# Optimization experiments

Hardware: AMD Instinct MI355X
Metric: run time of the kernel (lower is better)

## Reference

```python
import jax, jax.numpy as jnp
import numpy as np

N_NODES = 50000
N_EDGES = 150000
EMB = 64
IN_DIM = 32
LN_EPS = 1e-5


def setup_inputs() -> dict:
    key = jax.random.key(0)
    k1, k2, k3, k4 = jax.random.split(key, 4)
    h = jax.random.normal(k1, (N_NODES, EMB), dtype=jnp.float32)
    edge_attr = jax.random.normal(k2, (N_EDGES, IN_DIM), dtype=jnp.float32)
    edge_index = jax.random.randint(k3, (2, N_EDGES), 0, N_NODES, dtype=jnp.int64)
    # xavier_uniform for [EMB*EMB, IN_DIM] weight
    limit = float(np.sqrt(6.0 / (EMB * EMB + IN_DIM)))
    W = jax.random.uniform(k4, (EMB * EMB, IN_DIM), dtype=jnp.float32,
                           minval=-limit, maxval=limit)
    b = jnp.zeros((EMB * EMB,), dtype=jnp.float32)
    gamma = jnp.ones((EMB,), dtype=jnp.float32)
    beta = jnp.zeros((EMB,), dtype=jnp.float32)
    return {"h": h, "edge_attr": edge_attr, "W": W, "b": b,
            "gamma": gamma, "beta": beta, "edge_index": edge_index}


def reference(h, edge_attr, W, b, gamma, beta, edge_index):
    M = edge_attr.shape[0]
    E = h.shape[1]
    # per-edge transform matrix from edge features: [M, E, E]
    m = (edge_attr @ W.T + b).reshape(M, E, E)
    # gather target-node features and apply per-edge matvec: [M, E]
    h_j = h[edge_index[1]]
    msg = jnp.einsum('mef,mf->me', m, h_j)
    # scatter-add messages to source nodes
    aggr = jax.ops.segment_sum(msg, edge_index[0], num_segments=h.shape[0])
    # residual + LayerNorm
    x = h + aggr
    mu = jnp.mean(x, axis=-1, keepdims=True)
    var = jnp.mean(jnp.square(x - mu), axis=-1, keepdims=True)
    y = (x - mu) * jax.lax.rsqrt(var + LN_EPS)
    return y * gamma + beta
```

## Files before the change

kernel.cpp:

```cpp
#include <hip/hip_runtime.h>
#include <math.h>

#define N_NODES 50000
#define N_EDGES 150000
#define LN_EPS 1e-5f

#define BM 128
#define WM 64

typedef _Float16 f16x8 __attribute__((ext_vector_type(8)));
typedef float    f32x4 __attribute__((ext_vector_type(4)));

__global__ void prep_kernel(const float* __restrict__ W, const float* __restrict__ b,
                            _Float16* __restrict__ WtF) {
    int tid = blockIdx.x * 256 + threadIdx.x;
    if (tid >= 66 * 4 * 64 * 8) return;
    int i  = tid & 7;
    int l  = (tid >> 3) & 63;
    int nb = (tid >> 9) & 3;
    int c  = tid >> 11;
    int k  = ((l >> 4) << 3) + i;
    int e  = nb * 16 + (l & 15);
    float v;
    if (c < 64) v = W[(e * 64 + c) * 32 + k];
    else        v = b[e * 64 + (c - 64) * 32 + k];
    WtF[tid] = (_Float16)v;
}

__global__ void init_kernel(const float* __restrict__ h, float* __restrict__ out) {
    int tid = blockIdx.x * 256 + threadIdx.x;
    ((float4*)out)[tid] = ((const float4*)h)[tid];
}

__launch_bounds__(128, 2)
__global__ void edge_kernel(const float* __restrict__ ea,
                            const float* __restrict__ h,
                            const int*   __restrict__ ei,
                            const f16x8* __restrict__ WtF,
                            float* __restrict__ out)
{
    __shared__ float s_hj[BM][68];
    __shared__ int   s_src[BM];

    const int t = threadIdx.x;
    const int m_base = blockIdx.x * BM;

    {
        int gm = m_base + t;
        if (gm < N_EDGES) {
            s_src[t] = ei[gm];
            const float4* hr = (const float4*)&h[(size_t)ei[N_EDGES + gm] * 64];
            #pragma unroll
            for (int j = 0; j < 16; ++j)
                *(float4*)&s_hj[t][j * 4] = hr[j];
        } else {
            s_src[t] = -1;
            float4 z = make_float4(0.f, 0.f, 0.f, 0.f);
            #pragma unroll
            for (int j = 0; j < 16; ++j)
                *(float4*)&s_hj[t][j * 4] = z;
        }
    }

    const int lane = t & 63;
    const int w    = t >> 6;
    const int r16  = lane & 15;
    const int g    = lane >> 4;
    const int k0   = g * 8;
    const int row0 = w * WM;

    float eareg[4][8];
    #pragma unroll
    for (int a = 0; a < 4; ++a) {
        int gm = m_base + row0 + a * 16 + r16;
        if (gm < N_EDGES) {
            float4 v0 = *(const float4*)&ea[(size_t)gm * 32 + k0];
            float4 v1 = *(const float4*)&ea[(size_t)gm * 32 + k0 + 4];
            eareg[a][0] = v0.x; eareg[a][1] = v0.y; eareg[a][2] = v0.z; eareg[a][3] = v0.w;
            eareg[a][4] = v1.x; eareg[a][5] = v1.y; eareg[a][6] = v1.z; eareg[a][7] = v1.w;
        } else {
            #pragma unroll
            for (int i = 0; i < 8; ++i) eareg[a][i] = 0.f;
        }
    }

    f32x4 acc[4][4];
    #pragma unroll
    for (int a = 0; a < 4; ++a)
        #pragma unroll
        for (int nb = 0; nb < 4; ++nb)
            acc[a][nb] = (f32x4){0.f, 0.f, 0.f, 0.f};

    __syncthreads();

    f16x8 bcur[4], bnxt[4];
    float hc[4], hn[4];
    #pragma unroll
    for (int nb = 0; nb < 4; ++nb) bcur[nb] = WtF[nb * 64 + lane];
    #pragma unroll
    for (int a = 0; a < 4; ++a) hc[a] = s_hj[row0 + a * 16 + r16][0];

    for (int c2 = 0; c2 < 32; ++c2) {
        const int c = 2 * c2;
        #pragma unroll
        for (int nb = 0; nb < 4; ++nb) bnxt[nb] = WtF[((c + 1) * 4 + nb) * 64 + lane];
        #pragma unroll
        for (int a = 0; a < 4; ++a) hn[a] = s_hj[row0 + a * 16 + r16][c + 1];
        #pragma unroll
        for (int a = 0; a < 4; ++a) {
            f16x8 va;
            #pragma unroll
            for (int i = 0; i < 4; ++i) {
                auto p = __builtin_amdgcn_cvt_pkrtz(eareg[a][2 * i]     * hc[a],
                                                    eareg[a][2 * i + 1] * hc[a]);
                va[2 * i]     = (_Float16)p[0];
                va[2 * i + 1] = (_Float16)p[1];
            }
            #pragma unroll
            for (int nb = 0; nb < 4; ++nb)
                acc[a][nb] = __builtin_amdgcn_mfma_f32_16x16x32_f16(va, bcur[nb], acc[a][nb], 0, 0, 0);
        }
        #pragma unroll
        for (int nb = 0; nb < 4; ++nb) bcur[nb] = WtF[((c + 2) * 4 + nb) * 64 + lane];
        {
            const int cn = (c + 2 < 64) ? (c + 2) : 0;
            #pragma unroll
            for (int a = 0; a < 4; ++a) hc[a] = s_hj[row0 + a * 16 + r16][cn];
        }
        #pragma unroll
        for (int a = 0; a < 4; ++a) {
            f16x8 va;
            #pragma unroll
            for (int i = 0; i < 4; ++i) {
                auto p = __builtin_amdgcn_cvt_pkrtz(eareg[a][2 * i]     * hn[a],
                                                    eareg[a][2 * i + 1] * hn[a]);
                va[2 * i]     = (_Float16)p[0];
                va[2 * i + 1] = (_Float16)p[1];
            }
            #pragma unroll
            for (int nb = 0; nb < 4; ++nb)
                acc[a][nb] = __builtin_amdgcn_mfma_f32_16x16x32_f16(va, bnxt[nb], acc[a][nb], 0, 0, 0);
        }
    }

    #pragma unroll
    for (int nb = 0; nb < 4; ++nb) bnxt[nb] = WtF[(65 * 4 + nb) * 64 + lane];
    #pragma unroll
    for (int a = 0; a < 4; ++a) {
        f16x8 va;
        #pragma unroll
        for (int i = 0; i < 8; ++i) va[i] = (_Float16)s_hj[row0 + a * 16 + r16][k0 + i];
        #pragma unroll
        for (int nb = 0; nb < 4; ++nb)
            acc[a][nb] = __builtin_amdgcn_mfma_f32_16x16x32_f16(va, bcur[nb], acc[a][nb], 0, 0, 0);
    }
    #pragma unroll
    for (int a = 0; a < 4; ++a) {
        f16x8 va;
        #pragma unroll
        for (int i = 0; i < 8; ++i) va[i] = (_Float16)s_hj[row0 + a * 16 + r16][32 + k0 + i];
        #pragma unroll
        for (int nb = 0; nb < 4; ++nb)
            acc[a][nb] = __builtin_amdgcn_mfma_f32_16x16x32_f16(va, bnxt[nb], acc[a][nb], 0, 0, 0);
    }

    #pragma unroll
    for (int a = 0; a < 4; ++a) {
        #pragma unroll
        for (int r = 0; r < 4; ++r) {
            int srcn = s_src[row0 + a * 16 + g * 4 + r];
            if (srcn >= 0) {
                #pragma unroll
                for (int nb = 0; nb < 4; ++nb)
                    atomicAdd(&out[(size_t)srcn * 64 + nb * 16 + r16], acc[a][nb][r]);
            }
        }
    }
}

__global__ void ln_kernel(const float* __restrict__ gamma, const float* __restrict__ beta,
                          float* __restrict__ out) {
    int row = blockIdx.x * 4 + (threadIdx.x >> 6);
    int lane = threadIdx.x & 63;
    if (row >= N_NODES) return;
    float x = out[row * 64 + lane];
    float s = x;
    #pragma unroll
    for (int o = 32; o; o >>= 1) s += __shfl_xor(s, o);
    float mu = s * (1.0f / 64.0f);
    float d = x - mu;
    float v = d * d;
    #pragma unroll
    for (int o = 32; o; o >>= 1) v += __shfl_xor(v, o);
    float var = v * (1.0f / 64.0f);
    float r = rsqrtf(var + LN_EPS);
    out[row * 64 + lane] = d * r * gamma[lane] + beta[lane];
}

extern "C" void kernel_launch(void* const* d_in, const int* in_sizes, int n_in,
                              void* d_out, int out_size, void* d_ws, size_t ws_size,
                              hipStream_t stream) {
    const float* h     = (const float*)d_in[0];
    const float* ea    = (const float*)d_in[1];
    const float* W     = (const float*)d_in[2];
    const float* b     = (const float*)d_in[3];
    const float* gamma = (const float*)d_in[4];
    const float* beta  = (const float*)d_in[5];
    const int*   ei    = (const int*)d_in[6];
    float* out = (float*)d_out;

    _Float16* WtF = (_Float16*)d_ws;

    prep_kernel<<<528, 256, 0, stream>>>(W, b, WtF);
    init_kernel<<<(N_NODES * 64 / 4 + 255) / 256, 256, 0, stream>>>(h, out);
    edge_kernel<<<(N_EDGES + BM - 1) / BM, 128, 0, stream>>>(ea, h, ei, (const f16x8*)WtF, out);
    ln_kernel<<<(N_NODES + 3) / 4, 256, 0, stream>>>(gamma, beta, out);
}
```

Measured before the change: 171.4 us.

## Split edge tile across four waves and triple-buffer weight fragment loads

The edge kernel now runs 256 threads per 128-edge block, so each wave covers 32 rows instead of 64. This halves the per-thread accumulator and edge-feature register footprint, and launch bounds are raised to allow four blocks per CU. Weight fragments are now prefetched three steps ahead instead of two, which gives more latency hiding per MFMA. The prep kernel is also vectorized to write 8-half vectors per thread. The tradeoff is that each weight fragment is now loaded by twice as many waves, doubling L2/L1 traffic for the shared B operand.

Measured after the change: 165.7 us. 3.3% less time.

```diff
diff --git a/kernel.cpp b/kernel.cpp
--- a/kernel.cpp
+++ b/kernel.cpp
@@ -6,25 +6,28 @@
 #define LN_EPS 1e-5f
 
 #define BM 128
-#define WM 64
+#define WM 32
 
 typedef _Float16 f16x8 __attribute__((ext_vector_type(8)));
 typedef float    f32x4 __attribute__((ext_vector_type(4)));
 
 __global__ void prep_kernel(const float* __restrict__ W, const float* __restrict__ b,
-                            _Float16* __restrict__ WtF) {
+                            f16x8* __restrict__ WtF) {
     int tid = blockIdx.x * 256 + threadIdx.x;
-    if (tid >= 66 * 4 * 64 * 8) return;
-    int i  = tid & 7;
-    int l  = (tid >> 3) & 63;
-    int nb = (tid >> 9) & 3;
-    int c  = tid >> 11;
-    int k  = ((l >> 4) << 3) + i;
+    if (tid >= 66 * 4 * 64) return;
+    int l  = tid & 63;
+    int nb = (tid >> 6) & 3;
+    int c  = tid >> 8;
+    int k0 = (l >> 4) << 3;
     int e  = nb * 16 + (l & 15);
-    float v;
-    if (c < 64) v = W[(e * 64 + c) * 32 + k];
-    else        v = b[e * 64 + (c - 64) * 32 + k];
-    WtF[tid] = (_Float16)v;
+    const float* src = (c < 64) ? &W[(e * 64 + c) * 32 + k0]
+                                : &b[e * 64 + (c - 64) * 32 + k0];
+    float4 v0 = *(const float4*)src;
+    float4 v1 = *(const float4*)(src + 4);
+    f16x8 o;
+    o[0] = (_Float16)v0.x; o[1] = (_Float16)v0.y; o[2] = (_Float16)v0.z; o[3] = (_Float16)v0.w;
+    o[4] = (_Float16)v1.x; o[5] = (_Float16)v1.y; o[6] = (_Float16)v1.z; o[7] = (_Float16)v1.w;
+    WtF[tid] = o;
 }
 
 __global__ void init_kernel(const float* __restrict__ h, float* __restrict__ out) {
@@ -32,7 +35,7 @@
     ((float4*)out)[tid] = ((const float4*)h)[tid];
 }
 
-__launch_bounds__(128, 2)
+__launch_bounds__(256, 4)
 __global__ void edge_kernel(const float* __restrict__ ea,
                             const float* __restrict__ h,
                             const int*   __restrict__ ei,
@@ -46,19 +49,21 @@
     const int m_base = blockIdx.x * BM;
 
     {
-        int gm = m_base + t;
+        int row  = t >> 1;
+        int half = t & 1;
+        int gm   = m_base + row;
         if (gm < N_EDGES) {
-            s_src[t] = ei[gm];
-            const float4* hr = (const float4*)&h[(size_t)ei[N_EDGES + gm] * 64];
-            #pragma unroll
-            for (int j = 0; j < 16; ++j)
-                *(float4*)&s_hj[t][j * 4] = hr[j];
+            if (half == 0) s_src[row] = ei[gm];
+            const float4* hr = (const float4*)&h[(size_t)ei[N_EDGES + gm] * 64 + half * 32];
+            #pragma unroll
+            for (int j = 0; j < 8; ++j)
+                *(float4*)&s_hj[row][half * 32 + j * 4] = hr[j];
         } else {
-            s_src[t] = -1;
+            if (half == 0) s_src[row] = -1;
             float4 z = make_float4(0.f, 0.f, 0.f, 0.f);
             #pragma unroll
-            for (int j = 0; j < 16; ++j)
-                *(float4*)&s_hj[t][j * 4] = z;
+            for (int j = 0; j < 8; ++j)
+                *(float4*)&s_hj[row][half * 32 + j * 4] = z;
         }
     }
 
@@ -68,10 +73,12 @@
     const int g    = lane >> 4;
     const int k0   = g * 8;
     const int row0 = w * WM;
-
-    float eareg[4][8];
-    #pragma unroll
-    for (int a = 0; a < 4; ++a) {
+    const int rA   = row0 + r16;
+    const int rB   = row0 + 16 + r16;
+
+    float eareg[2][8];
+    #pragma unroll
+    for (int a = 0; a < 2; ++a) {
         int gm = m_base + row0 + a * 16 + r16;
         if (gm < N_EDGES) {
             float4 v0 = *(const float4*)&ea[(size_t)gm * 32 + k0];
@@ -84,88 +91,110 @@
         }
     }
 
-    f32x4 acc[4][4];
-    #pragma unroll
-    for (int a = 0; a < 4; ++a)
+    f32x4 acc[2][4];
+    #pragma unroll
+    for (int a = 0; a < 2; ++a)
         #pragma unroll
         for (int nb = 0; nb < 4; ++nb)
             acc[a][nb] = (f32x4){0.f, 0.f, 0.f, 0.f};
 
     __syncthreads();
 
-    f16x8 bcur[4], bnxt[4];
-    float hc[4], hn[4];
-    #pragma unroll
-    for (int nb = 0; nb < 4; ++nb) bcur[nb] = WtF[nb * 64 + lane];
-    #pragma unroll
-    for (int a = 0; a < 4; ++a) hc[a] = s_hj[row0 + a * 16 + r16][0];
-
-    for (int c2 = 0; c2 < 32; ++c2) {
-        const int c = 2 * c2;
-        #pragma unroll
-        for (int nb = 0; nb < 4; ++nb) bnxt[nb] = WtF[((c + 1) * 4 + nb) * 64 + lane];
-        #pragma unroll
-        for (int a = 0; a < 4; ++a) hn[a] = s_hj[row0 + a * 16 + r16][c + 1];
-        #pragma unroll
-        for (int a = 0; a < 4; ++a) {
+    f16x8 b0[4], b1[4], b2[4];
+    #pragma unroll
+    for (int nb = 0; nb < 4; ++nb) b0[nb] = WtF[(0 * 4 + nb) * 64 + lane];
+    #pragma unroll
+    for (int nb = 0; nb < 4; ++nb) b1[nb] = WtF[(1 * 4 + nb) * 64 + lane];
+    #pragma unroll
+    for (int nb = 0; nb < 4; ++nb) b2[nb] = WtF[(2 * 4 + nb) * 64 + lane];
+
+    float hc0 = s_hj[rA][0];
+    float hc1 = s_hj[rB][0];
+
+    auto step = [&](int c, f16x8* bb, bool loadnext) {
+        float hn0 = 0.f, hn1 = 0.f;
+        if (loadnext) { hn0 = s_hj[rA][c + 1]; hn1 = s_hj[rB][c + 1]; }
+        {
             f16x8 va;
             #pragma unroll
             for (int i = 0; i < 4; ++i) {
-                auto p = __builtin_amdgcn_cvt_pkrtz(eareg[a][2 * i]     * hc[a],
-                                                    eareg[a][2 * i + 1] * hc[a]);
-                va[2 * i]     = (_Float16)p[0];
-                va[2 * i + 1] = (_Float16)p[1];
+                auto p = __builtin_amdgcn_cvt_pkrtz(eareg[0][2 * i]     * hc0,
+                                                    eareg[0][2 * i + 1] * hc0);
+                va[2 * i] = (_Float16)p[0]; va[2 * i + 1] = (_Float16)p[1];
             }
             #pragma unroll
             for (int nb = 0; nb < 4; ++nb)
-                acc[a][nb] = __builtin_amdgcn_mfma_f32_16x16x32_f16(va, bcur[nb], acc[a][nb], 0, 0, 0);
-        }
-        #pragma unroll
-        for (int nb = 0; nb < 4; ++nb) bcur[nb] = WtF[((c + 2) * 4 + nb) * 64 + lane];
+                acc[0][nb] = __builtin_amdgcn_mfma_f32_16x16x32_f16(va, bb[nb], acc[0][nb], 0, 0, 0);
+        }
         {
-            const int cn = (c + 2 < 64) ? (c + 2) : 0;
-            #pragma unroll
-            for (int a = 0; a < 4; ++a) hc[a] = s_hj[row0 + a * 16 + r16][cn];
-        }
-        #pragma unroll
-        for (int a = 0; a < 4; ++a) {
             f16x8 va;
             #pragma unroll
             for (int i = 0; i < 4; ++i) {
-                auto p = __builtin_amdgcn_cvt_pkrtz(eareg[a][2 * i]     * hn[a],
-                                                    eareg[a][2 * i + 1] * hn[a]);
-                va[2 * i]     = (_Float16)p[0];
-                va[2 * i + 1] = (_Float16)p[1];
+                auto p = __builtin_amdgcn_cvt_pkrtz(eareg[1][2 * i]     * hc1,
+                                                    eareg[1][2 * i + 1] * hc1);
+                va[2 * i] = (_Float16)p[0]; va[2 * i + 1] = (_Float16)p[1];
             }
             #pragma unroll
             for (int nb = 0; nb < 4; ++nb)
-                acc[a][nb] = __builtin_amdgcn_mfma_f32_16x16x32_f16(va, bnxt[nb], acc[a][nb], 0, 0, 0);
-        }
-    }
-
-    #pragma unroll
-    for (int nb = 0; nb < 4; ++nb) bnxt[nb] = WtF[(65 * 4 + nb) * 64 + lane];
-    #pragma unroll
-    for (int a = 0; a < 4; ++a) {
+                acc[1][nb] = __builtin_amdgcn_mfma_f32_16x16x32_f16(va, bb[nb], acc[1][nb], 0, 0, 0);
+        }
+        hc0 = hn0; hc1 = hn1;
+    };
+
+    for (int c = 0; c < 63; c += 3) {
+        step(c, b0, true);
+        #pragma unroll
+        for (int nb = 0; nb < 4; ++nb) b0[nb] = WtF[((c + 3) * 4 + nb) * 64 + lane];
+        step(c + 1, b1, true);
+        #pragma unroll
+        for (int nb = 0; nb < 4; ++nb) b1[nb] = WtF[((c + 4) * 4 + nb) * 64 + lane];
+        step(c + 2, b2, true);
+        #pragma unroll
+        for (int nb = 0; nb < 4; ++nb) b2[nb] = WtF[((c + 5) * 4 + nb) * 64 + lane];
+    }
+    step(63, b0, false);
+
+    {
         f16x8 va;
         #pragma unroll
-        for (int i = 0; i < 8; ++i) va[i] = (_Float16)s_hj[row0 + a * 16 + r16][k0 + i];
-        #pragma unroll
-        for (int nb = 0; nb < 4; ++nb)
-            acc[a][nb] = __builtin_amdgcn_mfma_f32_16x16x32_f16(va, bcur[nb], acc[a][nb], 0, 0, 0);
-    }
-    #pragma unroll
-    for (int a = 0; a < 4; ++a) {
+        for (int i = 0; i < 4; ++i) {
+            auto p = __builtin_amdgcn_cvt_pkrtz(s_hj[rA][k0 + 2 * i], s_hj[rA][k0 + 2 * i + 1]);
+            va[2 * i] = (_Float16)p[0]; va[2 * i + 1] = (_Float16)p[1];
+        }
+        #pragma unroll
+        for (int nb = 0; nb < 4; ++nb)
+            acc[0][nb] = __builtin_amdgcn_mfma_f32_16x16x32_f16(va, b1[nb], acc[0][nb], 0, 0, 0);
+        #pragma unroll
+        for (int i = 0; i < 4; ++i) {
+            auto p = __builtin_amdgcn_cvt_pkrtz(s_hj[rB][k0 + 2 * i], s_hj[rB][k0 + 2 * i + 1]);
+            va[2 * i] = (_Float16)p[0]; va[2 * i + 1] = (_Float16)p[1];
+        }
+        #pragma unroll
+        for (int nb = 0; nb < 4; ++nb)
+            acc[1][nb] = __builtin_amdgcn_mfma_f32_16x16x32_f16(va, b1[nb], acc[1][nb], 0, 0, 0);
+    }
+    {
         f16x8 va;
         #pragma unroll
-        for (int i = 0; i < 8; ++i) va[i] = (_Float16)s_hj[row0 + a * 16 + r16][32 + k0 + i];
-        #pragma unroll
-        for (int nb = 0; nb < 4; ++nb)
-            acc[a][nb] = __builtin_amdgcn_mfma_f32_16x16x32_f16(va, bnxt[nb], acc[a][nb], 0, 0, 0);
-    }
-
-    #pragma unroll
-    for (int a = 0; a < 4; ++a) {
+        for (int i = 0; i < 4; ++i) {
+            auto p = __builtin_amdgcn_cvt_pkrtz(s_hj[rA][32 + k0 + 2 * i], s_hj[rA][32 + k0 + 2 * i + 1]);
+            va[2 * i] = (_Float16)p[0]; va[2 * i + 1] = (_Float16)p[1];
+        }
+        #pragma unroll
+        for (int nb = 0; nb < 4; ++nb)
+            acc[0][nb] = __builtin_amdgcn_mfma_f32_16x16x32_f16(va, b2[nb], acc[0][nb], 0, 0, 0);
+        #pragma unroll
+        for (int i = 0; i < 4; ++i) {
+            auto p = __builtin_amdgcn_cvt_pkrtz(s_hj[rB][32 + k0 + 2 * i], s_hj[rB][32 + k0 + 2 * i + 1]);
+            va[2 * i] = (_Float16)p[0]; va[2 * i + 1] = (_Float16)p[1];
+        }
+        #pragma unroll
+        for (int nb = 0; nb < 4; ++nb)
+            acc[1][nb] = __builtin_amdgcn_mfma_f32_16x16x32_f16(va, b2[nb], acc[1][nb], 0, 0, 0);
+    }
+
+    #pragma unroll
+    for (int a = 0; a < 2; ++a) {
         #pragma unroll
         for (int r = 0; r < 4; ++r) {
             int srcn = s_src[row0 + a * 16 + g * 4 + r];
@@ -209,10 +238,10 @@
     const int*   ei    = (const int*)d_in[6];
     float* out = (float*)d_out;
 
-    _Float16* WtF = (_Float16*)d_ws;
-
-    prep_kernel<<<528, 256, 0, stream>>>(W, b, WtF);
+    f16x8* WtF = (f16x8*)d_ws;
+
+    prep_kernel<<<66, 256, 0, stream>>>(W, b, WtF);
     init_kernel<<<(N_NODES * 64 / 4 + 255) / 256, 256, 0, stream>>>(h, out);
-    edge_kernel<<<(N_EDGES + BM - 1) / BM, 128, 0, stream>>>(ea, h, ei, (const f16x8*)WtF, out);
+    edge_kernel<<<(N_EDGES + BM - 1) / BM, 256, 0, stream>>>(ea, h, ei, WtF, out);
     ln_kernel<<<(N_NODES + 3) / 4, 256, 0, stream>>>(gamma, beta, out);
 }
```
